# Kernel optimization log

Measured on AMD Instinct MI355X. Metric: run time of the kernel, lower is better.

The kernel has to match this reference:

```python
import jax, jax.numpy as jnp
import numpy as np

B, T, HOP = 4, 200, 120
N = T * HOP
M1, A1 = 40, 5            # mcep_order+1, apdc_order+1
HID, COND = 256, 192
SR = 24000.0
ALPHA = 0.466             # frequency-warping for 24 kHz
PD = 4                    # Pade order
PADE = jnp.asarray([1.0, 0.4999273, 0.1067005, 0.00956526, 0.0003041358], jnp.float32)
SIGN = jnp.asarray([1.0, -1.0, 1.0, -1.0], jnp.float32)  # + for odd Pade tap index
F0_MEAN, F0_STD = 5.0, 0.25
MCEP_MEAN, MCEP_STD = 0.0, 1.0
APDC_MEAN, APDC_STD = 0.0, 1.0
NOISE_RATIO, SP_RATE, F0_RATE = 0.5, 1.0, 1.0


def mc2b(mc, a):
    """SPTK mc2b: mel-cepstrum -> MLSA filter coefficients (scan over order)."""
    mc_rev = jnp.moveaxis(mc, -1, 0)[::-1]  # [M1, B, T]
    def step(carry, c):
        b = c - a * carry
        return b, b
    _, bs = jax.lax.scan(step, jnp.zeros_like(mc_rev[0]), mc_rev)
    return jnp.moveaxis(bs[::-1], 0, -1)


def _mlsafir(x, b, d):
    # SPTK mlsafir, vectorized over the PD Pade taps.
    # x: [PD], b: [M1], d: [PD, M1+1]
    aa = 1.0 - ALPHA * ALPHA
    d1 = aa * x + ALPHA * d[:, 1]
    def step(prev, di):  # d_new[i] = d[i] + a*(d[i+1] - d_new[i-1]) : order recurrence
        d_i, d_ip1 = di
        new = d_i + ALPHA * (d_ip1 - prev)
        return new, new
    xs = (d[:, 2:M1].T, d[:, 3:M1 + 1].T)  # [M1-2, PD]
    _, dupd = jax.lax.scan(step, d1, xs)    # [M1-2, PD]
    y = jnp.einsum('mp,m->p', dupd, b[2:])
    # delay-line shift: new d = [x, d1, d1, dupd[2..M]]
    new_d = jnp.concatenate([x[:, None], d1[:, None], d1[:, None], dupd.T], axis=1)
    return y, new_d


def _mlsa_step(state, inp):
    d1a, d1b, d2, pt2 = state
    x, b = inp
    x = x * jnp.exp(b[0])           # gain
    # ---- stage 1 (uses b[1] only), SPTK mlsadf1 ----
    aa = 1.0 - ALPHA * ALPHA
    na = aa * d1b[:PD] + ALPHA * d1a[1:]
    npt = na * b[1]
    v1 = npt * PADE[1:]
    x1 = x + jnp.sum(v1 * SIGN)
    y1 = jnp.sum(v1) + x1
    d1a = jnp.concatenate([d1a[:1], na])
    d1b = jnp.concatenate([x1[None], npt])
    # ---- stage 2 (orders >= 2), SPTK mlsadf2 ----
    fy, d2 = _mlsafir(pt2[:PD], b, d2)
    v2 = fy * PADE[1:]
    x2 = y1 + jnp.sum(v2 * SIGN)
    y2 = jnp.sum(v2) + x2
    pt2 = jnp.concatenate([x2[None], fy])
    return (d1a, d1b, d2, pt2), y2


def mlsa_filter(exc, b_up):
    # exc: [N], b_up: [N, M1] -> filtered waveform [N]
    init = (jnp.zeros(PD + 1, jnp.float32), jnp.zeros(PD + 1, jnp.float32),
            jnp.zeros((PD, M1 + 1), jnp.float32), jnp.zeros(PD + 1, jnp.float32))
    _, y = jax.lax.scan(_mlsa_step, init, (exc, b_up))
    return y


def _forward(mceps, apdcs, frame_f0s, noise,
             Wm, bm, Wa, ba, Wf, bf, Wpa, bpa, Wpp, bpp,
             Wrp, brp, Wra, bra, Wap):
    # linear feature embed + sum
    hs = mceps @ Wm + bm + apdcs @ Wa + ba + frame_f0s @ Wf + bf   # [B,T,HID]
    ca = hs @ Wpa + bpa                                             # prenet_a cond [B,T,COND]
    cp = hs @ Wpp + bpp                                             # prenet_p cond
    # denorm (+ exp for log-f0)
    f0 = jnp.exp(frame_f0s[..., 0] * F0_STD + F0_MEAN) * F0_RATE    # [B,T]
    sp = mceps * MCEP_STD + MCEP_MEAN
    ap = apdcs * APDC_STD + APDC_MEAN
    # per-path mel-cepstra with prenet residuals
    mc_p = sp * SP_RATE + 0.1 * jnp.tanh(cp @ Wrp + brp)
    mc_a = sp * SP_RATE + 0.1 * jnp.tanh(ca @ Wra + bra) + ap @ Wap
    b_p = mc2b(mc_p, ALPHA)
    b_a = mc2b(mc_a, ALPHA)
    # excitation at sample rate
    f0_up = jnp.repeat(f0, HOP, axis=1)                             # [B,N]
    phase = jnp.cumsum(f0_up / SR, axis=1)
    w = jnp.floor(phase)
    wprev = jnp.concatenate([jnp.zeros_like(w[:, :1]), w[:, :-1]], axis=1)
    amp = jnp.sqrt(SR / jnp.maximum(f0_up, 1.0))
    pulse = jnp.where(w > wprev, amp, 0.0)
    exc_p = pulse * (1.0 - NOISE_RATIO)
    exc_a = noise * NOISE_RATIO
    # run both (periodic/aperiodic) MLSA synthesis filters in one batched scan
    excs = jnp.concatenate([exc_p, exc_a], axis=0)                  # [2B,N]
    bs = jnp.repeat(jnp.concatenate([b_p, b_a], axis=0), HOP, axis=1)  # [2B,N,M1]
    wavs = jax.vmap(mlsa_filter)(excs, bs)                          # [2B,N]
    return wavs[:B] + wavs[B:]


_forward_jit = jax.jit(_forward)


def setup_inputs() -> dict:
    key = jax.random.key(0)
    ks = jax.random.split(key, 20)
    decay = 0.3 / (1.0 + jnp.arange(M1, dtype=jnp.float32))  # realistic cepstral decay (filter stability)
    return {
        'mceps': jax.random.normal(ks[0], (B, T, M1), jnp.float32) * decay,
        'apdcs': jax.random.normal(ks[1], (B, T, A1), jnp.float32) * 0.3,
        'frame_f0s': jax.random.normal(ks[2], (B, T, 1), jnp.float32),
        'noise': jax.random.normal(ks[3], (B, N), jnp.float32),
        'Wm': jax.random.normal(ks[4], (M1, HID), jnp.float32) / np.sqrt(M1),
        'bm': jnp.zeros((HID,), jnp.float32),
        'Wa': jax.random.normal(ks[5], (A1, HID), jnp.float32) / np.sqrt(A1),
        'ba': jnp.zeros((HID,), jnp.float32),
        'Wf': jax.random.normal(ks[6], (1, HID), jnp.float32),
        'bf': jnp.zeros((HID,), jnp.float32),
        'Wpa': jax.random.normal(ks[7], (HID, COND), jnp.float32) / np.sqrt(HID),
        'bpa': jnp.zeros((COND,), jnp.float32),
        'Wpp': jax.random.normal(ks[8], (HID, COND), jnp.float32) / np.sqrt(HID),
        'bpp': jnp.zeros((COND,), jnp.float32),
        'Wrp': jax.random.normal(ks[9], (COND, M1), jnp.float32) / np.sqrt(COND),
        'brp': jnp.zeros((M1,), jnp.float32),
        'Wra': jax.random.normal(ks[10], (COND, M1), jnp.float32) / np.sqrt(COND),
        'bra': jnp.zeros((M1,), jnp.float32),
        'Wap': jax.random.normal(ks[11], (A1, M1), jnp.float32) * 0.05,
    }


def reference(mceps, apdcs, frame_f0s, noise,
              Wm, bm, Wa, ba, Wf, bf, Wpa, bpa, Wpp, bpp,
              Wrp, brp, Wra, bra, Wap):
    return _forward_jit(mceps, apdcs, frame_f0s, noise,
                        Wm, bm, Wa, ba, Wf, bf, Wpa, bpa, Wpp, bpp,
                        Wrp, brp, Wra, bra, Wap)
```

## Files before the change

### kernel.cpp

```cpp
#include <hip/hip_runtime.h>
#include <math.h>

#define ALPHA 0.466f
#define T_FRAMES 200
#define HOPW 120
#define NSAMP 24000
#define M1 40
#define HID 256
#define CONDW 192

#define NCHUNK 100
#define CHUNKF 2
#define WARMF 4
#define SERF (WARMF + CHUNKF)

#define F8 8
#define EMB_BLOCKS (4 * T_FRAMES / F8)
#define BPF ((NSAMP + 255) / 256)

__global__ __launch_bounds__(256) void prep_kernel(
    const float* __restrict__ mceps, const float* __restrict__ apdcs,
    const float* __restrict__ f0s, const float* __restrict__ noise,
    const float* __restrict__ Wm, const float* __restrict__ bm,
    const float* __restrict__ Wa, const float* __restrict__ ba,
    const float* __restrict__ Wf, const float* __restrict__ bf,
    const float* __restrict__ Wpa, const float* __restrict__ bpa,
    const float* __restrict__ Wpp, const float* __restrict__ bpp,
    const float* __restrict__ Wrp, const float* __restrict__ brp,
    const float* __restrict__ Wra, const float* __restrict__ bra,
    const float* __restrict__ Wap,
    float* __restrict__ bcoef, float* __restrict__ exc)
{
    const int tid = threadIdx.x;

    if (blockIdx.x >= EMB_BLOCKS) {
        const int xb = blockIdx.x - EMB_BLOCKS;
        const int ff = xb / BPF;
        const int n = (xb % BPF) * 256 + tid;

        if (ff >= 4) {
            if (n < NSAMP) exc[ff * NSAMP + n] = 0.5f * noise[(ff - 4) * NSAMP + n];
            return;
        }

        __shared__ double s_base[T_FRAMES];
        __shared__ double s_step[T_FRAMES];
        __shared__ float  s_amp[T_FRAMES];

        if (tid < 64) {
            const int L = tid;
            double st[4], loc[4];
            float am[4];
            double s = 0.0;
            #pragma unroll
            for (int j = 0; j < 4; ++j) {
                int ft = L * 4 + j;
                if (ft < T_FRAMES) {
                    double fv = exp((double)f0s[ff * T_FRAMES + ft] * 0.25 + 5.0);
                    st[j] = fv / 24000.0;
                    am[j] = (float)(0.5 * sqrt(24000.0 / fmax(fv, 1.0)));
                } else { st[j] = 0.0; am[j] = 0.f; }
                loc[j] = s;
                s += st[j];
            }
            double tot = s;
            #pragma unroll
            for (int off = 1; off < 64; off <<= 1) {
                double v = __shfl_up(s, off, 64);
                if (L >= off) s += v;
            }
            double excl = s - tot;
            #pragma unroll
            for (int j = 0; j < 4; ++j) {
                int ft = L * 4 + j;
                if (ft < T_FRAMES) {
                    s_base[ft] = 120.0 * (excl + loc[j]);
                    s_step[ft] = st[j];
                    s_amp[ft]  = am[j];
                }
            }
        }
        __syncthreads();

        if (n < NSAMP) {
            int ft = n / HOPW, k = n - ft * HOPW;
            double st = s_step[ft], bs = s_base[ft];
            double ph  = bs + (double)(k + 1) * st;
            double php = bs + (double)k * st;
            exc[ff * NSAMP + n] = (floor(ph) > floor(php)) ? s_amp[ft] : 0.0f;
        }
        return;
    }

    __shared__ float s_mc[F8][M1];
    __shared__ float s_ap[F8][5];
    __shared__ float s_f0[F8];
    __shared__ float s_h[F8][HID];
    __shared__ float s_ca[F8][CONDW];
    __shared__ float s_cp[F8][CONDW];
    __shared__ float s_mcp[F8][M1];
    __shared__ float s_mca[F8][M1];

    const int R0 = blockIdx.x * F8;

    for (int j = tid; j < F8 * M1; j += 256) s_mc[j / M1][j % M1] = mceps[R0 * M1 + j];
    if (tid < F8 * 5) s_ap[tid / 5][tid % 5] = apdcs[R0 * 5 + tid];
    if (tid < F8)     s_f0[tid] = f0s[R0 + tid];
    __syncthreads();

    {
        float acc[F8];
        const float bias = bm[tid] + ba[tid] + bf[tid];
        #pragma unroll
        for (int r = 0; r < F8; ++r) acc[r] = bias;
        for (int k = 0; k < M1; ++k) {
            float w = Wm[k * HID + tid];
            #pragma unroll
            for (int r = 0; r < F8; ++r) acc[r] = fmaf(s_mc[r][k], w, acc[r]);
        }
        #pragma unroll
        for (int k = 0; k < 5; ++k) {
            float w = Wa[k * HID + tid];
            #pragma unroll
            for (int r = 0; r < F8; ++r) acc[r] = fmaf(s_ap[r][k], w, acc[r]);
        }
        float wf = Wf[tid];
        #pragma unroll
        for (int r = 0; r < F8; ++r) s_h[r][tid] = fmaf(s_f0[r], wf, acc[r]);
    }
    __syncthreads();

    if (tid < CONDW) {
        float aA[F8], aP[F8];
        #pragma unroll
        for (int r = 0; r < F8; ++r) { aA[r] = bpa[tid]; aP[r] = bpp[tid]; }
        for (int k = 0; k < HID; k += 4) {
            float4 h4[F8];
            #pragma unroll
            for (int r = 0; r < F8; ++r) h4[r] = *(const float4*)&s_h[r][k];
            #pragma unroll
            for (int kk = 0; kk < 4; ++kk) {
                float wa = Wpa[(k + kk) * CONDW + tid];
                float wp = Wpp[(k + kk) * CONDW + tid];
                #pragma unroll
                for (int r = 0; r < F8; ++r) {
                    float hv = (&h4[r].x)[kk];
                    aA[r] = fmaf(hv, wa, aA[r]);
                    aP[r] = fmaf(hv, wp, aP[r]);
                }
            }
        }
        #pragma unroll
        for (int r = 0; r < F8; ++r) { s_ca[r][tid] = aA[r]; s_cp[r][tid] = aP[r]; }
    }
    __syncthreads();

    if (tid < M1) {
        const int u = tid;
        float acc[F8];
        #pragma unroll
        for (int r = 0; r < F8; ++r) acc[r] = brp[u];
        for (int k = 0; k < CONDW; k += 4) {
            float4 c4[F8];
            #pragma unroll
            for (int r = 0; r < F8; ++r) c4[r] = *(const float4*)&s_cp[r][k];
            #pragma unroll
            for (int kk = 0; kk < 4; ++kk) {
                float w = Wrp[(k + kk) * M1 + u];
                #pragma unroll
                for (int r = 0; r < F8; ++r) acc[r] = fmaf((&c4[r].x)[kk], w, acc[r]);
            }
        }
        #pragma unroll
        for (int r = 0; r < F8; ++r)
            s_mcp[r][u] = s_mc[r][u] + 0.1f * tanhf(acc[r]);
    } else if (tid >= 64 && tid < 64 + M1) {
        const int u = tid - 64;
        float acc[F8];
        #pragma unroll
        for (int r = 0; r < F8; ++r) acc[r] = bra[u];
        for (int k = 0; k < CONDW; k += 4) {
            float4 c4[F8];
            #pragma unroll
            for (int r = 0; r < F8; ++r) c4[r] = *(const float4*)&s_ca[r][k];
            #pragma unroll
            for (int kk = 0; kk < 4; ++kk) {
                float w = Wra[(k + kk) * M1 + u];
                #pragma unroll
                for (int r = 0; r < F8; ++r) acc[r] = fmaf((&c4[r].x)[kk], w, acc[r]);
            }
        }
        #pragma unroll
        for (int r = 0; r < F8; ++r) {
            float aw = 0.f;
            #pragma unroll
            for (int j = 0; j < 5; ++j) aw = fmaf(s_ap[r][j], Wap[j * M1 + u], aw);
            s_mca[r][u] = s_mc[r][u] + 0.1f * tanhf(acc[r]) + aw;
        }
    }
    __syncthreads();

    if (tid < 16) {
        const int r = tid >> 1, path = tid & 1;
        const int R = R0 + r;
        const int batch = R / T_FRAMES, t = R - batch * T_FRAMES;
        const float* src = path ? s_mca[r] : s_mcp[r];
        float* dst = bcoef + ((path * 4 + batch) * T_FRAMES + t) * M1;
        float prev = src[M1 - 1];
        dst[M1 - 1] = prev;
        for (int m = M1 - 2; m >= 0; --m) {
            prev = src[m] - ALPHA * prev;
            dst[m] = prev;
        }
    }
}

template <int CTRL>
__device__ __forceinline__ float rshr(float x) {
    return __int_as_float(
        __builtin_amdgcn_mov_dpp(__float_as_int(x), CTRL, 0xF, 0xF, true));
}
__device__ __forceinline__ float rlane(float x, int l) {
    return __int_as_float(__builtin_amdgcn_readlane(__float_as_int(x), l));
}

template <bool OUT>
__device__ __forceinline__ void run_frame(
    const float* __restrict__ sx, float AB,
    float BP1, float BP2, float BP3, float BP4,
    float Ba, float Bb, float Bc, float K, float IPw, int i16, int row,
    float& E0, float& E1, float& E2, float& dlp, float& xin,
    float& m1, float& m2, float& m3, float& m4, float& w0,
    float* __restrict__ ybuf)
{
    const float A = ALPHA;
    const float AA = 1.0f - A * A;
    const float A2 = A * A;
    const float R1 = -(A * A * A);
    const float R2 = R1 * R1;
    const float R4 = R2 * R2;
    const float R8 = R4 * R4;

    float xc = sx[0];
    #pragma unroll 8
    for (int k = 0; k < HOPW; ++k) {
        float xn = sx[k + 1];
        float x = xc;

        float na0 = AA * w0 + A * m1;
        float na1 = AB * m1 + A * m2;
        float na2 = AB * m2 + A * m3;
        float na3 = AB * m3 + A * m4;
        float v10 = na0 * BP1, v11 = na1 * BP2, v12 = na2 * BP3, v13 = na3 * BP4;
        float x1 = x + ((v10 - v11) + (v12 - v13));
        float y1 = ((v10 + v11) + (v12 + v13)) + x1;
        m1 = na0; m2 = na1; m3 = na2; m4 = na3; w0 = x1;

        float pE2 = rshr<0x111>(E2);
        float ca = fmaf(A, E0, (i16 == 0) ? dlp : pE2);
        float cb = fmaf(A, E1, E0);
        float cc = fmaf(A, E2, E1);
        float ua = ca;
        float ub = fmaf(-A, ua, cb);
        float uc = fmaf(-A, ub, cc);
        float X = uc;
        X = fmaf(R1, rshr<0x111>(X), X);
        X = fmaf(R2, rshr<0x112>(X), X);
        X = fmaf(R4, rshr<0x114>(X), X);
        X = fmaf(R8, rshr<0x118>(X), X);
        float dl = fmaf(AA, xin, A * dlp);
        float Xt = fmaf(K, dl, X);
        float Si = rshr<0x111>(Xt);
        Si = (i16 == 0) ? dl : Si;
        float ta = fmaf(-A, Si, ua);
        float tb = fmaf(A2, Si, ub);

        float fp = ta * Ba;
        fp = fmaf(tb, Bb, fp);
        fp = fmaf(Xt, Bc, fp);
        float S = fp;
        S += rshr<0x111>(S);
        S += rshr<0x112>(S);
        S += rshr<0x114>(S);
        S += rshr<0x118>(S);

        float xprev = rshr<0x142>(S) * IPw;

        float v20 = rlane(S, 15);
        float v21 = rlane(S, 31);
        float v22 = rlane(S, 47);
        float v23 = rlane(S, 63);
        float e = v20 + v22, o = v21 + v23;
        float x2 = y1 + (e - o);
        if (OUT) {
            float y2 = (e + o) + x2;
            ybuf[k] = y2;
        }

        xin = (row == 0) ? x2 : xprev;
        E0 = ta; E1 = tb; E2 = Xt;
        dlp = dl;
        xc = xn;
    }
}

__global__ __launch_bounds__(64) void mlsa_kernel(
    const float* __restrict__ bcoef, const float* __restrict__ exc,
    float* __restrict__ out)
{
    __shared__ float sexc[HOPW + 2];
    __shared__ float ybuf[HOPW];

    const int tid = threadIdx.x;
    const int i16 = tid & 15;
    const int row = tid >> 4;
    const int chunk = blockIdx.x >> 3;
    const int f = blockIdx.x & 7;
    const int b = f & 3;

    const float P1 = 0.4999273f, P2 = 0.1067005f, P3 = 0.00956526f, P4 = 0.0003041358f;
    const float Pw  = (row == 0) ? P1 : (row == 1) ? P2 : (row == 2) ? P3 : P4;
    const float IPw = (row == 1) ? (1.f / P1) : (row == 2) ? (1.f / P2) : (1.f / P3);

    const float R1 = -(ALPHA * ALPHA * ALPHA);
    float K = R1;
    for (int j = 0; j < i16; ++j) K *= R1;

    float E0 = 0.f, E1 = 0.f, E2 = 0.f;
    float dlp = 0.f, xin = 0.f;
    float m1 = 0.f, m2 = 0.f, m3 = 0.f, m4 = 0.f, w0 = 0.f;

    const int outF0 = chunk * CHUNKF;

    #pragma unroll 1
    for (int i = 0; i < SERF; ++i) {
        const int ftA = outF0 - WARMF + i;

        const int ftc = (ftA < 0) ? 0 : ftA;
        const float* bp = bcoef + (f * T_FRAMES + ftc) * M1;
        const float b1 = bp[1];
        const float G  = expf(bp[0]);
        const float AA = 1.0f - ALPHA * ALPHA;
        const float AB = AA * b1;
        const float BP1 = b1 * P1, BP2 = b1 * P2, BP3 = b1 * P3, BP4 = b1 * P4;

        for (int j = tid; j < HOPW; j += 64)
            sexc[j] = (ftA >= 0) ? exc[f * NSAMP + ftA * HOPW + j] * G : 0.f;
        if (tid == 0) sexc[HOPW] = 0.f;

        const int ja = 3 * i16 + 2;
        const float Ba = ((i16 <= 12) ? bp[ja]     : 0.f) * Pw;
        const float Bb = ((i16 <= 12) ? bp[ja + 1] : 0.f) * Pw;
        const float Bc = ((i16 <= 11) ? bp[ja + 2] : 0.f) * Pw;

        if (i >= WARMF) {
            run_frame<true>(sexc, AB, BP1, BP2, BP3, BP4, Ba, Bb, Bc, K, IPw,
                            i16, row, E0, E1, E2, dlp, xin, m1, m2, m3, m4, w0, ybuf);
            float* op = out + b * NSAMP + ftA * HOPW;
            atomicAdd(&op[tid], ybuf[tid]);
            if (tid < HOPW - 64) atomicAdd(&op[tid + 64], ybuf[tid + 64]);
        } else {
            run_frame<false>(sexc, AB, BP1, BP2, BP3, BP4, Ba, Bb, Bc, K, IPw,
                             i16, row, E0, E1, E2, dlp, xin, m1, m2, m3, m4, w0, ybuf);
        }
    }
}

extern "C" void kernel_launch(void* const* d_in, const int* in_sizes, int n_in,
                              void* d_out, int out_size, void* d_ws, size_t ws_size,
                              hipStream_t stream) {
    const float* mceps = (const float*)d_in[0];
    const float* apdcs = (const float*)d_in[1];
    const float* f0s   = (const float*)d_in[2];
    const float* noise = (const float*)d_in[3];
    const float* Wm  = (const float*)d_in[4];
    const float* bm  = (const float*)d_in[5];
    const float* Wa  = (const float*)d_in[6];
    const float* ba  = (const float*)d_in[7];
    const float* Wf  = (const float*)d_in[8];
    const float* bf  = (const float*)d_in[9];
    const float* Wpa = (const float*)d_in[10];
    const float* bpa = (const float*)d_in[11];
    const float* Wpp = (const float*)d_in[12];
    const float* bpp = (const float*)d_in[13];
    const float* Wrp = (const float*)d_in[14];
    const float* brp = (const float*)d_in[15];
    const float* Wra = (const float*)d_in[16];
    const float* bra = (const float*)d_in[17];
    const float* Wap = (const float*)d_in[18];
    float* out = (float*)d_out;

    char* ws = (char*)d_ws;
    float* bcoef = (float*)(ws + 0);
    float* exc   = (float*)(ws + 256000);

    hipMemsetAsync(out, 0, (size_t)out_size * sizeof(float), stream);

    prep_kernel<<<dim3(EMB_BLOCKS + 8 * BPF), dim3(256), 0, stream>>>(
        mceps, apdcs, f0s, noise, Wm, bm, Wa, ba, Wf, bf,
        Wpa, bpa, Wpp, bpp, Wrp, brp, Wra, bra, Wap, bcoef, exc);

    mlsa_kernel<<<dim3(NCHUNK * 8), dim3(64), 0, stream>>>(bcoef, exc, out);
}
```

Measured before the change: 220.5 us.

## Pack two MLSA streams per wavefront with 8 lanes per tap and direct stores

Each 64-lane block now runs both filter streams (periodic and aperiodic) for one batch item. Lanes alternate between streams, each lane holds 5 orders instead of 3, and the DPP shift/scan strides double to match. Frames per chunk drop from 2 to 1, so there are 200 chunks, and the two stream outputs are summed in shared memory and stored directly. This removes the atomicAdd and the memset. The per-lane serial work grows (5-order recurrence, extra readlanes and selects), and each chunk spends a larger share of its work on warm-up frames.

```diff
diff --git a/kernel.cpp b/kernel.cpp
--- a/kernel.cpp
+++ b/kernel.cpp
@@ -9,8 +9,8 @@
 #define HID 256
 #define CONDW 192
 
-#define NCHUNK 100
-#define CHUNKF 2
+#define NCHUNK 200
+#define CHUNKF 1
 #define WARMF 4
 #define SERF (WARMF + CHUNKF)
 
@@ -228,18 +228,21 @@
 __device__ __forceinline__ void run_frame(
     const float* __restrict__ sx, float AB,
     float BP1, float BP2, float BP3, float BP4,
-    float Ba, float Bb, float Bc, float K, float IPw, int i16, int row,
-    float& E0, float& E1, float& E2, float& dlp, float& xin,
+    float B0, float B1, float B2, float B3, float B4,
+    float K, float IPw, bool pos0, bool row0, bool parodd,
+    float& E0, float& E1, float& E2, float& E3, float& E4,
+    float& dlp, float& xin,
     float& m1, float& m2, float& m3, float& m4, float& w0,
-    float* __restrict__ ybuf)
+    float* __restrict__ yb)
 {
-    const float A = ALPHA;
-    const float AA = 1.0f - A * A;
-    const float A2 = A * A;
-    const float R1 = -(A * A * A);
-    const float R2 = R1 * R1;
-    const float R4 = R2 * R2;
-    const float R8 = R4 * R4;
+    const float A   = ALPHA;
+    const float AA  = 1.0f - A * A;
+    const float A2  = A * A;
+    const float mA3 = -(A * A2);
+    const float A4  = A2 * A2;
+    const float R   = -(A4 * A);
+    const float R2  = R * R;
+    const float R4  = R2 * R2;
 
     float xc = sx[0];
     #pragma unroll 8
@@ -247,58 +250,71 @@
         float xn = sx[k + 1];
         float x = xc;
 
-        float na0 = AA * w0 + A * m1;
-        float na1 = AB * m1 + A * m2;
-        float na2 = AB * m2 + A * m3;
-        float na3 = AB * m3 + A * m4;
-        float v10 = na0 * BP1, v11 = na1 * BP2, v12 = na2 * BP3, v13 = na3 * BP4;
-        float x1 = x + ((v10 - v11) + (v12 - v13));
-        float y1 = ((v10 + v11) + (v12 + v13)) + x1;
+        float na0 = fmaf(A, m1, AA * w0);
+        float na1 = fmaf(A, m2, AB * m1);
+        float na2 = fmaf(A, m3, AB * m2);
+        float na3 = fmaf(A, m4, AB * m3);
+        float p = fmaf(na2, BP3, na0 * BP1);
+        float q = fmaf(na3, BP4, na1 * BP2);
+        float x1 = x + (p - q);
+        float y1 = fmaf(2.0f, p, x);
         m1 = na0; m2 = na1; m3 = na2; m4 = na3; w0 = x1;
 
-        float pE2 = rshr<0x111>(E2);
-        float ca = fmaf(A, E0, (i16 == 0) ? dlp : pE2);
-        float cb = fmaf(A, E1, E0);
-        float cc = fmaf(A, E2, E1);
-        float ua = ca;
-        float ub = fmaf(-A, ua, cb);
-        float uc = fmaf(-A, ub, cc);
-        float X = uc;
-        X = fmaf(R1, rshr<0x111>(X), X);
-        X = fmaf(R2, rshr<0x112>(X), X);
-        X = fmaf(R4, rshr<0x114>(X), X);
-        X = fmaf(R8, rshr<0x118>(X), X);
+        float pE4 = rshr<0x112>(E4);
+        float c0 = fmaf(A, E0, pos0 ? dlp : pE4);
+        float c1 = fmaf(A, E1, E0);
+        float c2 = fmaf(A, E2, E1);
+        float c3 = fmaf(A, E3, E2);
+        float c4 = fmaf(A, E4, E3);
+        float u0 = c0;
+        float u1 = fmaf(-A, u0, c1);
+        float u2 = fmaf(-A, u1, c2);
+        float u3 = fmaf(-A, u2, c3);
+        float u4 = fmaf(-A, u3, c4);
+        float X = u4;
+        X = fmaf(R,  rshr<0x112>(X), X);
+        X = fmaf(R2, rshr<0x114>(X), X);
+        X = fmaf(R4, rshr<0x118>(X), X);
         float dl = fmaf(AA, xin, A * dlp);
         float Xt = fmaf(K, dl, X);
-        float Si = rshr<0x111>(Xt);
-        Si = (i16 == 0) ? dl : Si;
-        float ta = fmaf(-A, Si, ua);
-        float tb = fmaf(A2, Si, ub);
-
-        float fp = ta * Ba;
-        fp = fmaf(tb, Bb, fp);
-        fp = fmaf(Xt, Bc, fp);
+        float Si = rshr<0x112>(Xt);
+        Si = pos0 ? dl : Si;
+        float t0 = fmaf(-A,  Si, u0);
+        float t1 = fmaf(A2,  Si, u1);
+        float t2 = fmaf(mA3, Si, u2);
+        float t3 = fmaf(A4,  Si, u3);
+
+        float fp = t0 * B0;
+        fp = fmaf(t1, B1, fp);
+        fp = fmaf(t2, B2, fp);
+        fp = fmaf(t3, B3, fp);
+        fp = fmaf(Xt, B4, fp);
         float S = fp;
-        S += rshr<0x111>(S);
         S += rshr<0x112>(S);
         S += rshr<0x114>(S);
         S += rshr<0x118>(S);
 
-        float xprev = rshr<0x142>(S) * IPw;
-
-        float v20 = rlane(S, 15);
-        float v21 = rlane(S, 31);
-        float v22 = rlane(S, 47);
-        float v23 = rlane(S, 63);
-        float e = v20 + v22, o = v21 + v23;
-        float x2 = y1 + (e - o);
+        float Sx = rshr<0x111>(S);
+        float T1 = rshr<0x142>(S);
+        float T0 = rshr<0x142>(Sx);
+        float xprev = (parodd ? T1 : T0) * IPw;
+
+        float s0p = rlane(S, 14), s1p = rlane(S, 30);
+        float s2p = rlane(S, 46), s3p = rlane(S, 62);
+        float s0a = rlane(S, 15), s1a = rlane(S, 31);
+        float s2a = rlane(S, 47), s3a = rlane(S, 63);
+        float eP = s0p + s2p, oP = s1p + s3p;
+        float eA = s0a + s2a, oA = s1a + s3a;
+        float ce = parodd ? eA : eP;
+        float co = parodd ? oA : oP;
+        float x2 = y1 + (ce + co);
         if (OUT) {
-            float y2 = (e + o) + x2;
-            ybuf[k] = y2;
-        }
-
-        xin = (row == 0) ? x2 : xprev;
-        E0 = ta; E1 = tb; E2 = Xt;
+            float y2 = x2 + (ce - co);
+            yb[k] = y2;
+        }
+
+        xin = row0 ? x2 : xprev;
+        E0 = t0; E1 = t1; E2 = t2; E3 = t3; E4 = Xt;
         dlp = dl;
         xc = xn;
     }
@@ -308,60 +324,73 @@
     const float* __restrict__ bcoef, const float* __restrict__ exc,
     float* __restrict__ out)
 {
-    __shared__ float sexc[HOPW + 2];
-    __shared__ float ybuf[HOPW];
+    __shared__ float sexc[2][HOPW + 4];
+    __shared__ float ybuf[2][HOPW + 4];
 
     const int tid = threadIdx.x;
-    const int i16 = tid & 15;
+    const int par = tid & 1;
+    const int pos = (tid >> 1) & 7;
     const int row = tid >> 4;
-    const int chunk = blockIdx.x >> 3;
-    const int f = blockIdx.x & 7;
-    const int b = f & 3;
+    const int chunk = blockIdx.x >> 2;
+    const int b = blockIdx.x & 3;
+    const int f = par * 4 + b;
+    const bool pos0 = (pos == 0), row0 = (row == 0), parodd = (par != 0);
 
     const float P1 = 0.4999273f, P2 = 0.1067005f, P3 = 0.00956526f, P4 = 0.0003041358f;
-    const float Pw  = (row == 0) ? P1 : (row == 1) ? P2 : (row == 2) ? P3 : P4;
-    const float IPw = (row == 1) ? (1.f / P1) : (row == 2) ? (1.f / P2) : (1.f / P3);
-
-    const float R1 = -(ALPHA * ALPHA * ALPHA);
-    float K = R1;
-    for (int j = 0; j < i16; ++j) K *= R1;
-
-    float E0 = 0.f, E1 = 0.f, E2 = 0.f;
+    const float wrow = (row == 0) ? P1 : (row == 1) ? -P2 : (row == 2) ? P3 : -P4;
+    const float IPw  = (row == 1) ? (1.f / P1) : (row == 2) ? (-1.f / P2)
+                     : (row == 3) ? (1.f / P3) : 0.f;
+
+    const float A = ALPHA;
+    const float R = -(A * A * A * A * A);
+    float K = R;
+    for (int j = 0; j < pos; ++j) K *= R;
+
+    float E0 = 0.f, E1 = 0.f, E2 = 0.f, E3 = 0.f, E4 = 0.f;
     float dlp = 0.f, xin = 0.f;
     float m1 = 0.f, m2 = 0.f, m3 = 0.f, m4 = 0.f, w0 = 0.f;
 
-    const int outF0 = chunk * CHUNKF;
+    const float* sxp = sexc[par];
+    float* ybp = ybuf[par];
+    const int ja = 5 * pos + 2;
+    const int lh = tid >> 1;
 
     #pragma unroll 1
     for (int i = 0; i < SERF; ++i) {
-        const int ftA = outF0 - WARMF + i;
-
+        const int ftA = chunk - WARMF + i;
         const int ftc = (ftA < 0) ? 0 : ftA;
         const float* bp = bcoef + (f * T_FRAMES + ftc) * M1;
         const float b1 = bp[1];
         const float G  = expf(bp[0]);
-        const float AA = 1.0f - ALPHA * ALPHA;
-        const float AB = AA * b1;
+        const float AAc = 1.0f - A * A;
+        const float AB = AAc * b1;
         const float BP1 = b1 * P1, BP2 = b1 * P2, BP3 = b1 * P3, BP4 = b1 * P4;
 
-        for (int j = tid; j < HOPW; j += 64)
-            sexc[j] = (ftA >= 0) ? exc[f * NSAMP + ftA * HOPW + j] * G : 0.f;
-        if (tid == 0) sexc[HOPW] = 0.f;
-
-        const int ja = 3 * i16 + 2;
-        const float Ba = ((i16 <= 12) ? bp[ja]     : 0.f) * Pw;
-        const float Bb = ((i16 <= 12) ? bp[ja + 1] : 0.f) * Pw;
-        const float Bc = ((i16 <= 11) ? bp[ja + 2] : 0.f) * Pw;
+        const float* ex = exc + f * NSAMP + ftc * HOPW;
+        #pragma unroll
+        for (int m = 0; m < 4; ++m) {
+            int kk = lh + 32 * m;
+            if (kk < HOPW) sexc[par][kk] = (ftA >= 0) ? ex[kk] * G : 0.f;
+        }
+        if (tid < 2) sexc[tid][HOPW] = 0.f;
+
+        const float B0c = bp[ja]     * wrow;
+        const float B1c = bp[ja + 1] * wrow;
+        const float B2c = bp[ja + 2] * wrow;
+        const float B3c = (pos < 7) ? bp[ja + 3] * wrow : 0.f;
+        const float B4c = (pos < 7) ? bp[ja + 4] * wrow : 0.f;
 
         if (i >= WARMF) {
-            run_frame<true>(sexc, AB, BP1, BP2, BP3, BP4, Ba, Bb, Bc, K, IPw,
-                            i16, row, E0, E1, E2, dlp, xin, m1, m2, m3, m4, w0, ybuf);
-            float* op = out + b * NSAMP + ftA * HOPW;
-            atomicAdd(&op[tid], ybuf[tid]);
-            if (tid < HOPW - 64) atomicAdd(&op[tid + 64], ybuf[tid + 64]);
+            run_frame<true>(sxp, AB, BP1, BP2, BP3, BP4,
+                            B0c, B1c, B2c, B3c, B4c, K, IPw, pos0, row0, parodd,
+                            E0, E1, E2, E3, E4, dlp, xin, m1, m2, m3, m4, w0, ybp);
+            float* op = out + b * NSAMP + chunk * HOPW;
+            op[tid] = ybuf[0][tid] + ybuf[1][tid];
+            if (tid < HOPW - 64) op[tid + 64] = ybuf[0][tid + 64] + ybuf[1][tid + 64];
         } else {
-            run_frame<false>(sexc, AB, BP1, BP2, BP3, BP4, Ba, Bb, Bc, K, IPw,
-                             i16, row, E0, E1, E2, dlp, xin, m1, m2, m3, m4, w0, ybuf);
+            run_frame<false>(sxp, AB, BP1, BP2, BP3, BP4,
+                             B0c, B1c, B2c, B3c, B4c, K, IPw, pos0, row0, parodd,
+                             E0, E1, E2, E3, E4, dlp, xin, m1, m2, m3, m4, w0, ybp);
         }
     }
 }
@@ -394,11 +423,9 @@
     float* bcoef = (float*)(ws + 0);
     float* exc   = (float*)(ws + 256000);
 
-    hipMemsetAsync(out, 0, (size_t)out_size * sizeof(float), stream);
-
     prep_kernel<<<dim3(EMB_BLOCKS + 8 * BPF), dim3(256), 0, stream>>>(
         mceps, apdcs, f0s, noise, Wm, bm, Wa, ba, Wf, bf,
         Wpa, bpa, Wpp, bpp, Wrp, brp, Wra, bra, Wap, bcoef, exc);
 
-    mlsa_kernel<<<dim3(NCHUNK * 8), dim3(64), 0, stream>>>(bcoef, exc, out);
-}
+    mlsa_kernel<<<dim3(NCHUNK * 4), dim3(64), 0, stream>>>(bcoef, exc, out);
+}
```

After: 212.4 us. 3.7% less time.
